# Performance work log

Measured on AMD Instinct MI355X. Metric: run time of the kernel, lower is better.

Reference implementation:

```python
import jax, jax.numpy as jnp
import numpy as np

N = 100000   # nodes
D = 8        # in_dim/2 (per-node phase dim)
H = 256      # hidden_dim
E = 1600000  # directed edges (avg degree 16)


def setup_inputs() -> dict:
    key = jax.random.key(0)
    ks = jax.random.split(key, 8)
    q = jax.random.normal(ks[0], (N, D), jnp.float32)
    p = jax.random.normal(ks[1], (N, D), jnp.float32)
    # per-node diagonal positive-definite mass matrix (what get_mass() produces:
    # diag(relu(diag(.)) + 1e-4)); keep it well-conditioned for the inverse.
    m_diag = jax.random.uniform(ks[2], (N, D), jnp.float32) + 0.5
    M = jax.vmap(jnp.diag)(m_diag)  # [N, D, D]
    src = jax.random.randint(ks[3], (E,), 0, N, dtype=jnp.int32)
    off = jax.random.randint(ks[4], (E,), 1, N, dtype=jnp.int32)
    dst = ((src + off) % N).astype(jnp.int32)  # guaranteed no self-edges (euclid>0)
    W1 = jax.random.normal(ks[5], (D, H), jnp.float32) / jnp.sqrt(D)
    b1 = jnp.zeros((H,), jnp.float32)
    W2 = jax.random.normal(ks[6], (H, D), jnp.float32) / jnp.sqrt(H)
    b2 = jnp.zeros((D,), jnp.float32)
    gravity = jnp.ones((1, 1), jnp.float32)
    return {"q": q, "p": p, "M": M, "src": src, "dst": dst,
            "W1": W1, "b1": b1, "W2": W2, "b2": b2, "gravity": gravity}


def _gcn(x, src, dst, norm_src, norm_dst, W, b, n_nodes):
    # DGL GraphConv norm='both': D_out^{-1/2} on src, sum-aggregate, D_in^{-1/2} on dst
    m = (x * norm_src[:, None])[src]                       # [E, F]
    agg = jax.ops.segment_sum(m, dst, num_segments=n_nodes)
    return (agg * norm_dst[:, None]) @ W + b


def reference(q, p, M, src, dst, W1, b1, W2, b2, gravity):
    n = q.shape[0]
    ones_e = jnp.ones(src.shape[0], q.dtype)
    out_deg = jax.ops.segment_sum(ones_e, src, num_segments=n)
    in_deg = jax.ops.segment_sum(ones_e, dst, num_segments=n)
    norm_src = jnp.where(out_deg > 0, out_deg, 1.0) ** -0.5
    norm_dst = jnp.where(in_deg > 0, in_deg, 1.0) ** -0.5

    def P_scalar(qq):
        # ConvGNN: GraphConv -> ReLU -> GraphConv, residual add
        h = jax.nn.relu(_gcn(qq, src, dst, norm_src, norm_dst, W1, b1, n))
        h = _gcn(h, src, dst, norm_src, norm_dst, W2, b2, n) + qq      # [N, D]
        euclid = jnp.linalg.norm(h[src] - h[dst], axis=-1)             # [E]
        masses = M[src] * M[dst]                                       # [E, D, D]
        return 0.5 * jnp.sum(gravity[0, 0] * masses / euclid[:, None, None])

    # dHdq = grad of potential P w.r.t q (torch.autograd.grad in original)
    dHdQ = jax.grad(P_scalar)(q)
    # dHdp: per-node p_i @ inv(M_i)  (self-loop graph, degree 1 per node)
    dHdP = jnp.linalg.solve(jnp.swapaxes(M, -1, -2), p[..., None])[..., 0]
    return jnp.concatenate([dHdQ, dHdP], axis=-1)  # [N, 2D]
```

## Files before the change

### kernel.cpp

```cpp
#include <hip/hip_runtime.h>
#include <hip/hip_fp16.h>

#define DD 8
#define HH 256
#define CH 8192
#define PAYBITS 17
#define PAYMASK 0x1FFFF
#define FPITCH 20
#define BPITCH 28


typedef _Float16 h2f __attribute__((ext_vector_type(2)));

static __device__ __forceinline__ float dot2u(unsigned w, h2f z, float c) {
#if __has_builtin(__builtin_amdgcn_fdot2)
    return __builtin_amdgcn_fdot2(__builtin_bit_cast(h2f, w), z, c, false);
#else
    __half2 h = __builtin_bit_cast(__half2, w);
    float2 f = __half22float2(h);
    return fmaf(f.y, (float)z[1], fmaf(f.x, (float)z[0], c));
#endif
}
static __device__ __forceinline__ h2f pkh(float a, float b) {
    h2f r; r[0] = (_Float16)a; r[1] = (_Float16)b; return r;
}
static __device__ __forceinline__ unsigned pk2(float a, float b) {
    __half2 hh; hh.x = __float2half(a); hh.y = __float2half(b);
    return *(unsigned*)&hh;
}

template <int CTRL>
static __device__ __forceinline__ float dppadd(float x) {
    int y = __builtin_amdgcn_update_dpp(0, __builtin_bit_cast(int, x),
                                        CTRL, 0xF, 0xF, true);
    return x + __builtin_bit_cast(float, y);
}
static __device__ __forceinline__ void red16(float a[8]) {
#pragma unroll
    for (int k = 0; k < 8; k++) a[k] = dppadd<0xB1>(a[k]);
#pragma unroll
    for (int k = 0; k < 8; k++) a[k] = dppadd<0x4E>(a[k]);
#pragma unroll
    for (int k = 0; k < 8; k++) a[k] = dppadd<0x141>(a[k]);
#pragma unroll
    for (int k = 0; k < 8; k++) a[k] = dppadd<0x140>(a[k]);
}
static __device__ __forceinline__ void red8(float a[8]) {
#pragma unroll
    for (int k = 0; k < 8; k++) a[k] = dppadd<0xB1>(a[k]);
#pragma unroll
    for (int k = 0; k < 8; k++) a[k] = dppadd<0x4E>(a[k]);
#pragma unroll
    for (int k = 0; k < 8; k++) a[k] = dppadd<0x141>(a[k]);
}


__global__ void k_coarse(const int* __restrict__ src, const int* __restrict__ dst,
                         int* __restrict__ gHistIn, int* __restrict__ gHistOut,
                         int NB, int E) {
    __shared__ int hIn[256], hOut[256];
    if (threadIdx.x < 256) { hIn[threadIdx.x] = 0; hOut[threadIdx.x] = 0; }
    __syncthreads();
    int lo = blockIdx.x * CH;
    int hi = min(lo + CH, E);
    for (int i = lo + threadIdx.x; i < hi; i += blockDim.x) {
        atomicAdd(&hIn[dst[i] >> 9], 1);
        atomicAdd(&hOut[src[i] >> 9], 1);
    }
    __syncthreads();
    if (threadIdx.x < NB) {
        int ci = hIn[threadIdx.x], co = hOut[threadIdx.x];
        if (ci) atomicAdd(&gHistIn[threadIdx.x], ci);
        if (co) atomicAdd(&gHistOut[threadIdx.x], co);
    }
}

__global__ void k_cscan(const int* __restrict__ gHistIn, const int* __restrict__ gHistOut,
                        int* __restrict__ cStartIn, int* __restrict__ cStartOut,
                        int* __restrict__ cCurIn, int* __restrict__ cCurOut,
                        int NB, int E) {
    __shared__ int s[256];
#pragma unroll
    for (int dir = 0; dir < 2; dir++) {
        const int* gh = dir ? gHistOut : gHistIn;
        int* cs = dir ? cStartOut : cStartIn;
        int* cc = dir ? cCurOut : cCurIn;
        int v = (threadIdx.x < NB) ? gh[threadIdx.x] : 0;
        s[threadIdx.x] = v;
        __syncthreads();
        for (int off = 1; off < 256; off <<= 1) {
            int t = (threadIdx.x >= off) ? s[threadIdx.x - off] : 0;
            __syncthreads();
            s[threadIdx.x] += t;
            __syncthreads();
        }
        if (threadIdx.x < NB) {
            int ex = s[threadIdx.x] - v;
            cs[threadIdx.x] = ex;
            cc[threadIdx.x] = ex;
        }
        if (threadIdx.x == 0) cs[NB] = E;
        __syncthreads();
    }
}

__global__ void k_part2(const int* __restrict__ src, const int* __restrict__ dst,
                        int* __restrict__ cCurIn, int* __restrict__ cCurOut,
                        int* __restrict__ P_in, int* __restrict__ P_out,
                        int NB, int E) {
    int dir = blockIdx.y;
    const int* key = dir ? src : dst;
    const int* pay = dir ? dst : src;
    int* cCur = dir ? cCurOut : cCurIn;
    int* P    = dir ? P_out   : P_in;
    __shared__ int h[256];
    if (threadIdx.x < 256) h[threadIdx.x] = 0;
    __syncthreads();
    int lo = blockIdx.x * CH;
    int hi = min(lo + CH, E);
    for (int i = lo + threadIdx.x; i < hi; i += blockDim.x)
        atomicAdd(&h[key[i] >> 9], 1);
    __syncthreads();
    if (threadIdx.x < NB) {
        int c = h[threadIdx.x];
        h[threadIdx.x] = c ? atomicAdd(&cCur[threadIdx.x], c) : 0;
    }
    __syncthreads();
    for (int i = lo + threadIdx.x; i < hi; i += blockDim.x) {
        int k = key[i];
        int pos = atomicAdd(&h[k >> 9], 1);
        P[pos] = ((k & 511) << PAYBITS) | pay[i];
    }
}

__launch_bounds__(512)
__global__ void k_fine2(const int* __restrict__ cStartIn, const int* __restrict__ cStartOut,
                        const int* __restrict__ P_in, const int* __restrict__ P_out,
                        int* __restrict__ start_in, int* __restrict__ start_out,
                        int* __restrict__ csr_in, int* __restrict__ csr_out, int N) {
    int dir = blockIdx.y;
    const int* cStart = dir ? cStartOut : cStartIn;
    const int* P      = dir ? P_out     : P_in;
    int* start        = dir ? start_out : start_in;
    int* csr          = dir ? csr_out   : csr_in;
    __shared__ int cnt[512], scn[512];
    int b = blockIdx.x;
    int lo = cStart[b], hi = cStart[b + 1];
    cnt[threadIdx.x] = 0;
    __syncthreads();
    for (int i = lo + threadIdx.x; i < hi; i += 512)
        atomicAdd(&cnt[P[i] >> PAYBITS], 1);
    __syncthreads();
    int own = cnt[threadIdx.x];
    scn[threadIdx.x] = own;
    __syncthreads();
    for (int off = 1; off < 512; off <<= 1) {
        int t = (threadIdx.x >= off) ? scn[threadIdx.x - off] : 0;
        __syncthreads();
        scn[threadIdx.x] += t;
        __syncthreads();
    }
    int base = lo + scn[threadIdx.x] - own;
    int node = (b << 9) + threadIdx.x;
    if (node < N) start[node] = base;
    cnt[threadIdx.x] = base;
    __syncthreads();
    for (int i = lo + threadIdx.x; i < hi; i += 512) {
        int p = P[i];
        int pos = atomicAdd(&cnt[p >> PAYBITS], 1);
        csr[pos] = p & PAYMASK;
    }
}

__global__ void k_prep(const float* __restrict__ q, const float* __restrict__ p,
                       const float* __restrict__ M,
                       const float* __restrict__ W1, const float* __restrict__ W2,
                       unsigned* __restrict__ Fp, unsigned* __restrict__ Bp,
                       int* __restrict__ start_in, int* __restrict__ start_out,
                       float* __restrict__ a, float* __restrict__ b,
                       __half2* __restrict__ hm, __half* __restrict__ qn,
                       float* __restrict__ out, int N, int E) {
    int t = blockIdx.x * blockDim.x + threadIdx.x;
    if (t == 0) { start_in[N] = E; start_out[N] = E; }
    if (t < 128) {
        int ci = t >> 4, l16 = t & 15;
        int j0 = ci * 32 + l16, j1 = j0 + 16;
        unsigned* F = Fp + t * FPITCH;
        unsigned* B = Bp + t * BPITCH;
#pragma unroll
        for (int k = 0; k < 4; k++) {
            unsigned c0 = pk2(W1[(2 * k) * HH + j0], W1[(2 * k + 1) * HH + j0]);
            unsigned c1 = pk2(W1[(2 * k) * HH + j1], W1[(2 * k + 1) * HH + j1]);
            F[k] = c0; F[4 + k] = c1; B[k] = c0; B[4 + k] = c1;
        }
#pragma unroll
        for (int k = 0; k < 8; k++)
            F[8 + k] = pk2(W2[j0 * DD + k], W2[j1 * DD + k]);
#pragma unroll
        for (int kk = 0; kk < 4; kk++) {
            B[8 + kk]  = pk2(W2[j0 * DD + 2 * kk], W2[j0 * DD + 2 * kk + 1]);
            B[12 + kk] = pk2(W2[j1 * DD + 2 * kk], W2[j1 * DD + 2 * kk + 1]);
        }
#pragma unroll
        for (int d = 0; d < 8; d++)
            B[16 + d] = pk2(W1[d * HH + j0], W1[d * HH + j1]);
        B[24] = 0; B[25] = 0; B[26] = 0; B[27] = 0;
    }
    int v = t;
    if (v >= N) return;
    int ei1 = (v + 1 < N) ? start_in[v + 1]  : E;
    int eo1 = (v + 1 < N) ? start_out[v + 1] : E;
    float din  = (float)(ei1 - start_in[v]);
    float dout = (float)(eo1 - start_out[v]);
    float av = 1.0f / sqrtf(dout > 0.f ? dout : 1.f);
    float bv = 1.0f / sqrtf(din  > 0.f ? din  : 1.f);
    a[v] = av; b[v] = bv;
#pragma unroll
    for (int d = 0; d < DD; d++) {
        float m = M[(size_t)v * DD * DD + d * (DD + 1)];
        __half2 hmv;
        hmv.x = __float2half(0.f);
        hmv.y = __float2half(m);
        hm[(size_t)v * DD + d] = hmv;
        qn[(size_t)v * DD + d] = __float2half(av * q[(size_t)v * DD + d]);
        out[(size_t)v * 2 * DD + DD + d] = p[(size_t)v * DD + d] / m;
    }
}

static __device__ __forceinline__
void acc_h8(uint4 r, float acc[8]) {
    float2 f;
    f = __half22float2(*(__half2*)&r.x); acc[0] += f.x; acc[1] += f.y;
    f = __half22float2(*(__half2*)&r.y); acc[2] += f.x; acc[3] += f.y;
    f = __half22float2(*(__half2*)&r.z); acc[4] += f.x; acc[5] += f.y;
    f = __half22float2(*(__half2*)&r.w); acc[6] += f.x; acc[7] += f.y;
}

static __device__ __forceinline__
void unpack_hm(uint4 r0, uint4 r1, float h[8], float m[8]) {
    float2 f;
    f = __half22float2(*(__half2*)&r0.x); h[0] = f.x; m[0] = f.y;
    f = __half22float2(*(__half2*)&r0.y); h[1] = f.x; m[1] = f.y;
    f = __half22float2(*(__half2*)&r0.z); h[2] = f.x; m[2] = f.y;
    f = __half22float2(*(__half2*)&r0.w); h[3] = f.x; m[3] = f.y;
    f = __half22float2(*(__half2*)&r1.x); h[4] = f.x; m[4] = f.y;
    f = __half22float2(*(__half2*)&r1.y); h[5] = f.x; m[5] = f.y;
    f = __half22float2(*(__half2*)&r1.z); h[6] = f.x; m[6] = f.y;
    f = __half22float2(*(__half2*)&r1.w); h[7] = f.x; m[7] = f.y;
}

static __device__ __forceinline__
void gather_h8(const int* __restrict__ csr, const __half* __restrict__ x,
               int e, int e1, float acc[8]) {
    for (; e + 3 < e1; e += 4) {
        int u0 = csr[e], u1 = csr[e + 1], u2 = csr[e + 2], u3 = csr[e + 3];
        uint4 r0 = *(const uint4*)(x + (size_t)u0 * DD);
        uint4 r1 = *(const uint4*)(x + (size_t)u1 * DD);
        uint4 r2 = *(const uint4*)(x + (size_t)u2 * DD);
        uint4 r3 = *(const uint4*)(x + (size_t)u3 * DD);
        acc_h8(r0, acc); acc_h8(r1, acc); acc_h8(r2, acc); acc_h8(r3, acc);
    }
    for (; e < e1; e++) {
        uint4 r = *(const uint4*)(x + (size_t)csr[e] * DD);
        acc_h8(r, acc);
    }
}

__launch_bounds__(256)
__global__ void k_agg_mlp_fwd(const int* __restrict__ start, const int* __restrict__ csr,
                              const __half* __restrict__ qn,
                              const float* __restrict__ a, const float* __restrict__ b,
                              const unsigned* __restrict__ Fp, const float* __restrict__ b1,
                              float* __restrict__ agg1, __half* __restrict__ ya, int N) {
    __shared__ unsigned sF[128 * FPITCH];
    __shared__ float sb1[HH];
    for (int i = threadIdx.x; i < 128 * FPITCH; i += 256) sF[i] = Fp[i];
    for (int i = threadIdx.x; i < HH; i += 256) sb1[i] = b1[i];
    __syncthreads();
    int t = blockIdx.x * 256 + threadIdx.x;
    int v = t >> 4, l16 = t & 15, sub = (t >> 3) & 1, d = t & 7;
    if (v >= N) return;
    int e0 = start[v], e1 = start[v + 1];
    float ag[DD] = {0.f, 0.f, 0.f, 0.f, 0.f, 0.f, 0.f, 0.f};
    for (int e = e0 + l16; e < e1; e += 16) {
        uint4 r = *(const uint4*)(qn + (size_t)csr[e] * DD);
        acc_h8(r, ag);
    }
    red16(ag);
    if (l16 < 2) {
        float4 val = l16 ? make_float4(ag[4], ag[5], ag[6], ag[7])
                         : make_float4(ag[0], ag[1], ag[2], ag[3]);
        ((float4*)(agg1 + (size_t)v * DD))[l16] = val;
    }
    float bv = b[v];
    h2f zh[4];
#pragma unroll
    for (int k = 0; k < 4; k++) zh[k] = pkh(bv * ag[2 * k], bv * ag[2 * k + 1]);
    float acc[DD] = {0.f, 0.f, 0.f, 0.f, 0.f, 0.f, 0.f, 0.f};
#pragma unroll
    for (int ci = 0; ci < 8; ci++) {
        int pid = ci * 16 + l16;
        const uint4* pw = (const uint4*)(sF + pid * FPITCH);
        uint4 w1a = pw[0], w1b = pw[1], w2p0 = pw[2], w2p1 = pw[3];
        int j0 = ci * 32 + l16;
        float u0 = sb1[j0], u1 = sb1[j0 + 16];
        u0 = dot2u(w1a.x, zh[0], u0); u0 = dot2u(w1a.y, zh[1], u0);
        u0 = dot2u(w1a.z, zh[2], u0); u0 = dot2u(w1a.w, zh[3], u0);
        u1 = dot2u(w1b.x, zh[0], u1); u1 = dot2u(w1b.y, zh[1], u1);
        u1 = dot2u(w1b.z, zh[2], u1); u1 = dot2u(w1b.w, zh[3], u1);
        h2f hh = pkh(fmaxf(u0, 0.f), fmaxf(u1, 0.f));
        acc[0] = dot2u(w2p0.x, hh, acc[0]); acc[1] = dot2u(w2p0.y, hh, acc[1]);
        acc[2] = dot2u(w2p0.z, hh, acc[2]); acc[3] = dot2u(w2p0.w, hh, acc[3]);
        acc[4] = dot2u(w2p1.x, hh, acc[4]); acc[5] = dot2u(w2p1.y, hh, acc[5]);
        acc[6] = dot2u(w2p1.z, hh, acc[6]); acc[7] = dot2u(w2p1.w, hh, acc[7]);
    }
    red16(acc);
    float yl = acc[0];
#pragma unroll
    for (int k = 1; k < DD; k++) yl = (d == k) ? acc[k] : yl;
    if (!sub) ya[(size_t)v * DD + d] = __float2half(a[v] * yl);
}

__launch_bounds__(256)
__global__ void k_h_node(const int* __restrict__ start, const int* __restrict__ csr,
                         const __half* __restrict__ ya, const float* __restrict__ b,
                         const float* __restrict__ q, const float* __restrict__ b2,
                         __half2* __restrict__ hm, int N) {
    int t = blockIdx.x * 256 + threadIdx.x;
    int v = t >> 3, sub = t & 7;
    if (v >= N) return;
    int e0 = start[v], e1 = start[v + 1], len = e1 - e0;
    int lo = e0 + (len * sub) / 8, hi = e0 + (len * (sub + 1)) / 8;
    float acc[8] = {0.f, 0.f, 0.f, 0.f, 0.f, 0.f, 0.f, 0.f};
    gather_h8(csr, ya, lo, hi, acc);
    red8(acc);
    if (sub == 0) {
        float bv = b[v];
        const float4* qp = (const float4*)(q + (size_t)v * DD);
        float4 q0 = qp[0], q1 = qp[1];
        float hq[8] = {q0.x, q0.y, q0.z, q0.w, q1.x, q1.y, q1.z, q1.w};
        __half2* hp = hm + (size_t)v * DD;
#pragma unroll
        for (int k = 0; k < DD; k++) {
            float hval = fmaf(bv, acc[k], b2[k] + hq[k]);
            __half2 cur = hp[k];
            cur.x = __float2half(hval);
            hp[k] = cur;
        }
    }
}

__launch_bounds__(256)
__global__ void k_gh4(const int* __restrict__ start_in, const int* __restrict__ csr_in,
                      const int* __restrict__ start_out, const int* __restrict__ csr_out,
                      const __half2* __restrict__ hm,
                      const float* __restrict__ b, const float* __restrict__ grav,
                      float* __restrict__ gh, __half* __restrict__ bgh, int N) {
    int t = blockIdx.x * 256 + threadIdx.x;
    int v = t >> 3, sub = t & 7, dir = sub >> 2, qr = sub & 3;
    if (v >= N) return;
    const uint4* srec = (const uint4*)(hm + (size_t)v * DD);
    uint4 s0 = srec[0], s1 = srec[1];
    float hv[8], mv[8];
    unpack_hm(s0, s1, hv, mv);
    const int* start = dir ? start_out : start_in;
    const int* csr   = dir ? csr_out   : csr_in;
    int e0 = start[v], e1 = start[v + 1], len = e1 - e0;
    int e  = e0 + (len * qr) / 4;
    int hi = e0 + (len * (qr + 1)) / 4;
    float coef = -0.5f * grav[0];
    float acc[8] = {0.f, 0.f, 0.f, 0.f, 0.f, 0.f, 0.f, 0.f};
    for (; e + 1 < hi; e += 2) {
        int u0 = csr[e], u1 = csr[e + 1];
        const uint4* r0p = (const uint4*)(hm + (size_t)u0 * DD);
        const uint4* r1p = (const uint4*)(hm + (size_t)u1 * DD);
        uint4 x0 = r0p[0], x1 = r0p[1], y0 = r1p[0], y1 = r1p[1];
        float hu0[8], mu0[8], hu1[8], mu1[8];
        unpack_hm(x0, x1, hu0, mu0);
        unpack_hm(y0, y1, hu1, mu1);
        float d0[8], d1[8];
        float e20 = 0.f, S0 = 0.f, e21 = 0.f, S1 = 0.f;
#pragma unroll
        for (int k = 0; k < 8; k++) {
            d0[k] = hv[k] - hu0[k];
            d1[k] = hv[k] - hu1[k];
            e20 = fmaf(d0[k], d0[k], e20);
            e21 = fmaf(d1[k], d1[k], e21);
            S0 = fmaf(mv[k], mu0[k], S0);
            S1 = fmaf(mv[k], mu1[k], S1);
        }
        float r0 = rsqrtf(e20), r1 = rsqrtf(e21);
        float c0 = coef * S0 * r0 * r0 * r0;
        float c1 = coef * S1 * r1 * r1 * r1;
#pragma unroll
        for (int k = 0; k < 8; k++)
            acc[k] = fmaf(c0, d0[k], fmaf(c1, d1[k], acc[k]));
    }
    if (e < hi) {
        int u = csr[e];
        const uint4* rp = (const uint4*)(hm + (size_t)u * DD);
        uint4 x0 = rp[0], x1 = rp[1];
        float hu[8], mu[8];
        unpack_hm(x0, x1, hu, mu);
        float df[8];
        float e2 = 0.f, S = 0.f;
#pragma unroll
        for (int k = 0; k < 8; k++) {
            df[k] = hv[k] - hu[k];
            e2 = fmaf(df[k], df[k], e2);
            S = fmaf(mv[k], mu[k], S);
        }
        float r = rsqrtf(e2);
        float c = coef * S * r * r * r;
#pragma unroll
        for (int k = 0; k < 8; k++) acc[k] = fmaf(c, df[k], acc[k]);
    }
    red8(acc);
    if (sub == 0) {
        float4* gp = (float4*)(gh + (size_t)v * DD);
        gp[0] = make_float4(acc[0], acc[1], acc[2], acc[3]);
        gp[1] = make_float4(acc[4], acc[5], acc[6], acc[7]);
        float bv = b[v];
        __half2* bp = (__half2*)(bgh + (size_t)v * DD);
        bp[0] = __floats2half2_rn(bv * acc[0], bv * acc[1]);
        bp[1] = __floats2half2_rn(bv * acc[2], bv * acc[3]);
        bp[2] = __floats2half2_rn(bv * acc[4], bv * acc[5]);
        bp[3] = __floats2half2_rn(bv * acc[6], bv * acc[7]);
    }
}

__launch_bounds__(256)
__global__ void k_bgh_mlp_bwd(const int* __restrict__ start, const int* __restrict__ csr,
                              const __half* __restrict__ bgh,
                              const float* __restrict__ agg1,
                              const float* __restrict__ a, const float* __restrict__ b,
                              const unsigned* __restrict__ Bp, const float* __restrict__ b1,
                              __half* __restrict__ gz1b, int N) {
    __shared__ unsigned sB[128 * BPITCH];
    __shared__ float sb1[HH];
    for (int i = threadIdx.x; i < 128 * BPITCH; i += 256) sB[i] = Bp[i];
    for (int i = threadIdx.x; i < HH; i += 256) sb1[i] = b1[i];
    __syncthreads();
    int t = blockIdx.x * 256 + threadIdx.x;
    int v = t >> 4, l16 = t & 15, sub = (t >> 3) & 1, d = t & 7;
    if (v >= N) return;
    int e0 = start[v], e1 = start[v + 1];
    float gq[DD] = {0.f, 0.f, 0.f, 0.f, 0.f, 0.f, 0.f, 0.f};
    for (int e = e0 + l16; e < e1; e += 16) {
        uint4 r = *(const uint4*)(bgh + (size_t)csr[e] * DD);
        acc_h8(r, gq);
    }
    red16(gq);
    float bv = b[v], av = a[v];
    const float4* ap = (const float4*)(agg1 + (size_t)v * DD);
    float4 a0 = ap[0], a1 = ap[1];
    h2f zh[4], gqh[4];
    zh[0] = pkh(bv * a0.x, bv * a0.y); zh[1] = pkh(bv * a0.z, bv * a0.w);
    zh[2] = pkh(bv * a1.x, bv * a1.y); zh[3] = pkh(bv * a1.z, bv * a1.w);
#pragma unroll
    for (int k = 0; k < 4; k++) gqh[k] = pkh(gq[2 * k], gq[2 * k + 1]);
    float gz[DD] = {0.f, 0.f, 0.f, 0.f, 0.f, 0.f, 0.f, 0.f};
#pragma unroll
    for (int ci = 0; ci < 8; ci++) {
        int pid = ci * 16 + l16;
        const uint4* pw = (const uint4*)(sB + pid * BPITCH);
        uint4 w1a = pw[0], w1b = pw[1], w2r0 = pw[2], w2r1 = pw[3];
        uint4 g0p = pw[4], g1p = pw[5];
        int j0 = ci * 32 + l16;
        float u0 = sb1[j0], u1 = sb1[j0 + 16];
        u0 = dot2u(w1a.x, zh[0], u0); u0 = dot2u(w1a.y, zh[1], u0);
        u0 = dot2u(w1a.z, zh[2], u0); u0 = dot2u(w1a.w, zh[3], u0);
        u1 = dot2u(w1b.x, zh[0], u1); u1 = dot2u(w1b.y, zh[1], u1);
        u1 = dot2u(w1b.z, zh[2], u1); u1 = dot2u(w1b.w, zh[3], u1);
        float ga0 = dot2u(w2r0.x, gqh[0], 0.f);
        ga0 = dot2u(w2r0.y, gqh[1], ga0);
        ga0 = dot2u(w2r0.z, gqh[2], ga0);
        ga0 = dot2u(w2r0.w, gqh[3], ga0);
        float ga1 = dot2u(w2r1.x, gqh[0], 0.f);
        ga1 = dot2u(w2r1.y, gqh[1], ga1);
        ga1 = dot2u(w2r1.z, gqh[2], ga1);
        ga1 = dot2u(w2r1.w, gqh[3], ga1);
        float g0 = (u0 > 0.f) ? av * ga0 : 0.f;
        float g1 = (u1 > 0.f) ? av * ga1 : 0.f;
        h2f gg = pkh(g0, g1);
        gz[0] = dot2u(g0p.x, gg, gz[0]); gz[1] = dot2u(g0p.y, gg, gz[1]);
        gz[2] = dot2u(g0p.z, gg, gz[2]); gz[3] = dot2u(g0p.w, gg, gz[3]);
        gz[4] = dot2u(g1p.x, gg, gz[4]); gz[5] = dot2u(g1p.y, gg, gz[5]);
        gz[6] = dot2u(g1p.z, gg, gz[6]); gz[7] = dot2u(g1p.w, gg, gz[7]);
    }
    red16(gz);
    float out_l = gz[0];
#pragma unroll
    for (int k = 1; k < DD; k++) out_l = (d == k) ? gz[k] : out_l;
    if (!sub) gz1b[(size_t)v * DD + d] = __float2half(bv * out_l);
}

__launch_bounds__(256)
__global__ void k_out_node(const int* __restrict__ start, const int* __restrict__ csr,
                           const __half* __restrict__ gz1b, const float* __restrict__ gh,
                           const float* __restrict__ a, float* __restrict__ out, int N) {
    int t = blockIdx.x * 256 + threadIdx.x;
    int v = t >> 3, sub = t & 7;
    if (v >= N) return;
    int e0 = start[v], e1 = start[v + 1], len = e1 - e0;
    int lo = e0 + (len * sub) / 8, hi = e0 + (len * (sub + 1)) / 8;
    float acc[8] = {0.f, 0.f, 0.f, 0.f, 0.f, 0.f, 0.f, 0.f};
    gather_h8(csr, gz1b, lo, hi, acc);
    red8(acc);
    if (sub == 0) {
        float av = a[v];
        const float4* gp = (const float4*)(gh + (size_t)v * DD);
        float4 g0 = gp[0], g1 = gp[1];
        float4* op = (float4*)(out + (size_t)v * 2 * DD);
        op[0] = make_float4(fmaf(av, acc[0], g0.x), fmaf(av, acc[1], g0.y),
                            fmaf(av, acc[2], g0.z), fmaf(av, acc[3], g0.w));
        op[1] = make_float4(fmaf(av, acc[4], g1.x), fmaf(av, acc[5], g1.y),
                            fmaf(av, acc[6], g1.z), fmaf(av, acc[7], g1.w));
    }
}


extern "C" void kernel_launch(void* const* d_in, const int* in_sizes, int n_in,
                              void* d_out, int out_size, void* d_ws, size_t ws_size,
                              hipStream_t stream) {
    const float* q    = (const float*)d_in[0];
    const float* p    = (const float*)d_in[1];
    const float* M    = (const float*)d_in[2];
    const int*   src  = (const int*)d_in[3];
    const int*   dst  = (const int*)d_in[4];
    const float* W1   = (const float*)d_in[5];
    const float* b1   = (const float*)d_in[6];
    const float* W2   = (const float*)d_in[7];
    const float* b2   = (const float*)d_in[8];
    const float* grav = (const float*)d_in[9];
    float* out = (float*)d_out;

    int N = in_sizes[0] / DD;
    int E = in_sizes[3];
    size_t n = (size_t)N;
    int NB = (N + 511) >> 9;

    float*   ws   = (float*)d_ws;
    float*   a_   = ws;
    float*   b_   = ws + n;
    __half*  qn   = (__half*)(ws + 2 * n);
    float*   agg1 = ws + 10 * n;
    float*   gh   = ws + 18 * n;
    __half2* hm   = (__half2*)(ws + 26 * n);
    __half*  ya   = (__half*)(ws + 34 * n);
    __half*  bgh  = (__half*)(ws + 38 * n);
    __half*  gz1b = (__half*)(ws + 42 * n);

    int* iw        = (int*)(ws + 46 * n);
    int* csr_in    = iw;
    int* csr_out   = iw + (size_t)E;
    int* start_in  = iw + 2 * (size_t)E;
    int* start_out = start_in + n + 1;
    int* gHistIn   = start_out + n + 1;
    int* gHistOut  = gHistIn + 256;
    int* cStartIn  = gHistOut + 256;
    int* cStartOut = cStartIn + NB + 1;
    int* cCurIn    = cStartOut + NB + 1;
    int* cCurOut   = cCurIn + NB;
    int* iwEnd     = cCurOut + NB;
    unsigned* Fp   = (unsigned*)iwEnd;
    unsigned* Bp   = Fp + 128 * FPITCH;
    int* intAfter  = (int*)(Bp + 128 * BPITCH);
    int* P_in  = (E <= 16 * (long long)n) ? (int*)ws            : intAfter;
    int* P_out = (E <= 16 * (long long)n) ? (int*)(ws + 16 * n) : intAfter + E;

    hipMemsetAsync(gHistIn, 0, 512 * sizeof(int), stream);

    const int tb = 256;
    int gbN  = (N + tb - 1) / tb;
    int gb8  = (int)((8 * n + tb - 1) / tb);
    int gb16 = (int)((16 * n + tb - 1) / tb);
    int gbC  = (E + CH - 1) / CH;

    k_coarse  <<<gbC, tb, 0, stream>>>(src, dst, gHistIn, gHistOut, NB, E);
    k_cscan   <<<1, 256, 0, stream>>>(gHistIn, gHistOut, cStartIn, cStartOut,
                                      cCurIn, cCurOut, NB, E);
    k_part2   <<<dim3(gbC, 2), tb, 0, stream>>>(src, dst, cCurIn, cCurOut,
                                                P_in, P_out, NB, E);
    k_fine2   <<<dim3(NB, 2), 512, 0, stream>>>(cStartIn, cStartOut, P_in, P_out,
                                                start_in, start_out, csr_in, csr_out, N);
    k_prep    <<<gbN, tb, 0, stream>>>(q, p, M, W1, W2, Fp, Bp, start_in, start_out,
                                       a_, b_, hm, qn, out, N, E);

    k_agg_mlp_fwd<<<gb16, tb, 0, stream>>>(start_in, csr_in, qn, a_, b_,
                                           Fp, b1, agg1, ya, N);
    k_h_node  <<<gb8, tb, 0, stream>>>(start_in, csr_in, ya, b_, q, b2, hm, N);
    k_gh4     <<<gb8, tb, 0, stream>>>(start_in, csr_in, start_out, csr_out,
                                       hm, b_, grav, gh, bgh, N);
    k_bgh_mlp_bwd<<<gb16, tb, 0, stream>>>(start_out, csr_out, bgh, agg1, a_, b_,
                                           Bp, b1, gz1b, N);
    k_out_node<<<gb8, tb, 0, stream>>>(start_out, csr_out, gz1b, gh, a_, out, N);
}
```

Measured before the change: 302.9 us.

## Store per-chunk coarse histograms and scan them to avoid recounting in partition

The coarse histogram kernel now writes one histogram per edge chunk instead of atomically merging into a global one. The scan kernel computes a per-chunk exclusive base for every bucket, so the partition kernel no longer has to recount keys or do global atomic reservations. This removes one full pass over the keys plus the memset. In exchange the single-block scan kernel loops serially over all chunks twice per direction, and the partition order becomes deterministic.

```diff
diff --git a/kernel.cpp b/kernel.cpp
--- a/kernel.cpp
+++ b/kernel.cpp
@@ -56,10 +56,10 @@
 
 
 __global__ void k_coarse(const int* __restrict__ src, const int* __restrict__ dst,
-                         int* __restrict__ gHistIn, int* __restrict__ gHistOut,
-                         int NB, int E) {
+                         int* __restrict__ cHistIn, int* __restrict__ cHistOut,
+                         int E) {
     __shared__ int hIn[256], hOut[256];
-    if (threadIdx.x < 256) { hIn[threadIdx.x] = 0; hOut[threadIdx.x] = 0; }
+    hIn[threadIdx.x] = 0; hOut[threadIdx.x] = 0;
     __syncthreads();
     int lo = blockIdx.x * CH;
     int hi = min(lo + CH, E);
@@ -68,64 +68,55 @@
         atomicAdd(&hOut[src[i] >> 9], 1);
     }
     __syncthreads();
-    if (threadIdx.x < NB) {
-        int ci = hIn[threadIdx.x], co = hOut[threadIdx.x];
-        if (ci) atomicAdd(&gHistIn[threadIdx.x], ci);
-        if (co) atomicAdd(&gHistOut[threadIdx.x], co);
-    }
-}
-
-__global__ void k_cscan(const int* __restrict__ gHistIn, const int* __restrict__ gHistOut,
+    cHistIn [blockIdx.x * 256 + threadIdx.x] = hIn[threadIdx.x];
+    cHistOut[blockIdx.x * 256 + threadIdx.x] = hOut[threadIdx.x];
+}
+
+__global__ void k_cscan(int* __restrict__ cHistIn, int* __restrict__ cHistOut,
                         int* __restrict__ cStartIn, int* __restrict__ cStartOut,
-                        int* __restrict__ cCurIn, int* __restrict__ cCurOut,
-                        int NB, int E) {
+                        int NB, int NC, int E) {
     __shared__ int s[256];
+    int tid = threadIdx.x;
 #pragma unroll
     for (int dir = 0; dir < 2; dir++) {
-        const int* gh = dir ? gHistOut : gHistIn;
+        int* cH = dir ? cHistOut : cHistIn;
         int* cs = dir ? cStartOut : cStartIn;
-        int* cc = dir ? cCurOut : cCurIn;
-        int v = (threadIdx.x < NB) ? gh[threadIdx.x] : 0;
-        s[threadIdx.x] = v;
+        int tot = 0;
+        for (int c = 0; c < NC; c++) tot += cH[c * 256 + tid];
+        s[tid] = tot;
         __syncthreads();
         for (int off = 1; off < 256; off <<= 1) {
-            int t = (threadIdx.x >= off) ? s[threadIdx.x - off] : 0;
+            int t = (tid >= off) ? s[tid - off] : 0;
             __syncthreads();
-            s[threadIdx.x] += t;
+            s[tid] += t;
             __syncthreads();
         }
-        if (threadIdx.x < NB) {
-            int ex = s[threadIdx.x] - v;
-            cs[threadIdx.x] = ex;
-            cc[threadIdx.x] = ex;
-        }
-        if (threadIdx.x == 0) cs[NB] = E;
+        int run = s[tid] - tot;
+        if (tid < NB) cs[tid] = run;
+        if (tid == NB || (tid == 255 && NB > 255)) cs[NB] = E;
+        if (tid == 0) cs[NB] = E;
+        for (int c = 0; c < NC; c++) {
+            int h = cH[c * 256 + tid];
+            cH[c * 256 + tid] = run;
+            run += h;
+        }
         __syncthreads();
     }
 }
 
 __global__ void k_part2(const int* __restrict__ src, const int* __restrict__ dst,
-                        int* __restrict__ cCurIn, int* __restrict__ cCurOut,
-                        int* __restrict__ P_in, int* __restrict__ P_out,
-                        int NB, int E) {
+                        const int* __restrict__ cBaseIn, const int* __restrict__ cBaseOut,
+                        int* __restrict__ P_in, int* __restrict__ P_out, int E) {
     int dir = blockIdx.y;
-    const int* key = dir ? src : dst;
-    const int* pay = dir ? dst : src;
-    int* cCur = dir ? cCurOut : cCurIn;
-    int* P    = dir ? P_out   : P_in;
+    const int* key   = dir ? src : dst;
+    const int* pay   = dir ? dst : src;
+    const int* cBase = dir ? cBaseOut : cBaseIn;
+    int* P           = dir ? P_out    : P_in;
     __shared__ int h[256];
-    if (threadIdx.x < 256) h[threadIdx.x] = 0;
+    h[threadIdx.x] = cBase[blockIdx.x * 256 + threadIdx.x];
     __syncthreads();
     int lo = blockIdx.x * CH;
     int hi = min(lo + CH, E);
-    for (int i = lo + threadIdx.x; i < hi; i += blockDim.x)
-        atomicAdd(&h[key[i] >> 9], 1);
-    __syncthreads();
-    if (threadIdx.x < NB) {
-        int c = h[threadIdx.x];
-        h[threadIdx.x] = c ? atomicAdd(&cCur[threadIdx.x], c) : 0;
-    }
-    __syncthreads();
     for (int i = lo + threadIdx.x; i < hi; i += blockDim.x) {
         int k = key[i];
         int pos = atomicAdd(&h[k >> 9], 1);
@@ -539,6 +530,7 @@
     int E = in_sizes[3];
     size_t n = (size_t)N;
     int NB = (N + 511) >> 9;
+    int NC = (E + CH - 1) / CH;
 
     float*   ws   = (float*)d_ws;
     float*   a_   = ws;
@@ -556,32 +548,27 @@
     int* csr_out   = iw + (size_t)E;
     int* start_in  = iw + 2 * (size_t)E;
     int* start_out = start_in + n + 1;
-    int* gHistIn   = start_out + n + 1;
-    int* gHistOut  = gHistIn + 256;
-    int* cStartIn  = gHistOut + 256;
+    int* cStartIn  = start_out + n + 1;
     int* cStartOut = cStartIn + NB + 1;
-    int* cCurIn    = cStartOut + NB + 1;
-    int* cCurOut   = cCurIn + NB;
-    int* iwEnd     = cCurOut + NB;
+    int* iwEnd     = cStartOut + NB + 1;
     unsigned* Fp   = (unsigned*)iwEnd;
     unsigned* Bp   = Fp + 128 * FPITCH;
-    int* intAfter  = (int*)(Bp + 128 * BPITCH);
+    int* cHistIn   = (int*)(Bp + 128 * BPITCH);
+    int* cHistOut  = cHistIn + (size_t)NC * 256;
+    int* intAfter  = cHistOut + (size_t)NC * 256;
     int* P_in  = (E <= 16 * (long long)n) ? (int*)ws            : intAfter;
     int* P_out = (E <= 16 * (long long)n) ? (int*)(ws + 16 * n) : intAfter + E;
-
-    hipMemsetAsync(gHistIn, 0, 512 * sizeof(int), stream);
 
     const int tb = 256;
     int gbN  = (N + tb - 1) / tb;
     int gb8  = (int)((8 * n + tb - 1) / tb);
     int gb16 = (int)((16 * n + tb - 1) / tb);
-    int gbC  = (E + CH - 1) / CH;
-
-    k_coarse  <<<gbC, tb, 0, stream>>>(src, dst, gHistIn, gHistOut, NB, E);
-    k_cscan   <<<1, 256, 0, stream>>>(gHistIn, gHistOut, cStartIn, cStartOut,
-                                      cCurIn, cCurOut, NB, E);
-    k_part2   <<<dim3(gbC, 2), tb, 0, stream>>>(src, dst, cCurIn, cCurOut,
-                                                P_in, P_out, NB, E);
+
+    k_coarse  <<<NC, tb, 0, stream>>>(src, dst, cHistIn, cHistOut, E);
+    k_cscan   <<<1, 256, 0, stream>>>(cHistIn, cHistOut, cStartIn, cStartOut,
+                                      NB, NC, E);
+    k_part2   <<<dim3(NC, 2), tb, 0, stream>>>(src, dst, cHistIn, cHistOut,
+                                               P_in, P_out, E);
     k_fine2   <<<dim3(NB, 2), 512, 0, stream>>>(cStartIn, cStartOut, P_in, P_out,
                                                 start_in, start_out, csr_in, csr_out, N);
     k_prep    <<<gbN, tb, 0, stream>>>(q, p, M, W1, W2, Fp, Bp, start_in, start_out,
```

After: 371.9 us. 22.8% more time.
